# Performance work log

Measured on AMD Instinct MI355X. Metric: run time of the kernel, lower is better.

The kernel has to match this reference:

```python
import jax
import jax.numpy as jnp
import numpy as np

SIGMA = 0.5
COLLISION_WEIGHT = 100.0
CE_WEIGHTS = (1.0, 30.0, 30.0, 10.0)
B, V, F, P = 512, 778, 1538, 1024


def _cone_field(tri, pts):
    # Conical distance field of receiver triangle `tri` [B,P,3,3] evaluated at
    # intruder vertices `pts` [B,P,3,3] (Tzionas et al. penetration field,
    # penalize_outside=False, point2plane=False). Returns [B,P].
    c = tri.mean(axis=-2)                                   # triangle center [B,P,3]
    n = jnp.cross(tri[..., 1, :] - tri[..., 0, :], tri[..., 2, :] - tri[..., 0, :])
    n = n / (jnp.linalg.norm(n, axis=-1, keepdims=True) + 1e-9)
    d = pts - c[..., None, :]                               # [B,P,3,3]
    h = jnp.einsum('bpvc,bpc->bpv', d, n)                   # signed height along normal
    rho2 = jnp.maximum(jnp.sum(d * d, axis=-1) - h * h, 0.0)  # squared radial dist
    phi = jax.nn.relu(-h) * jnp.exp(-rho2 / (2.0 * SIGMA * SIGMA))
    return phi.sum(axis=-1)


def _pen_distance(triangles, collision_idxs):
    # triangles [B,2F,3,3]; collision_idxs [B,P,2] with -1 padding -> per-batch loss [B]
    bb = jnp.arange(triangles.shape[0])[:, None]
    valid = (collision_idxs[..., 0] >= 0) & (collision_idxs[..., 1] >= 0)
    idx = jnp.maximum(collision_idxs, 0)
    recv = triangles[bb, idx[..., 0]]                       # [B,P,3,3]
    intr = triangles[bb, idx[..., 1]]
    pair = _cone_field(recv, intr) + _cone_field(intr, recv)
    return jnp.sum(pair * valid, axis=1)


def _collision_loss(out_vertices, faces, collision_idxs):
    nv = out_vertices.shape[2]
    verts = jnp.concatenate([out_vertices[0], out_vertices[1]], axis=1)   # [B,2V,3]
    faces_comb = jnp.concatenate([faces[0], faces[1] + nv], axis=0)       # [2F,3]
    triangles = verts[:, faces_comb]                                      # [B,2F,3,3]
    loss_b = _pen_distance(triangles, collision_idxs)
    nz = (loss_b != 0).astype(loss_b.dtype)
    cnt = nz.sum()
    return jnp.where(cnt > 0, (loss_b * nz).sum() / jnp.maximum(cnt, 1.0) * COLLISION_WEIGHT, 0.0)


def _index_loss(elem, mask):
    # masked mean exactly as Loss.index_losss: sum(loss*mask)/ (mask.sum()*D), 0 if empty
    l = elem.reshape(elem.shape[0], -1)
    denom = mask.sum() * l.shape[1]
    return jnp.where(denom > 0, (l * mask[:, None]).sum() / jnp.maximum(denom, 1.0), 0.0)


def _mse(a, b):
    return (a - b) ** 2


def _l1(a, b):
    return jnp.abs(a - b)


def setup_inputs():
    key = jax.random.key(0)
    ks = jax.random.split(key, 20)
    f32 = jnp.float32
    out_vertices = jax.random.normal(ks[0], (2, B, V, 3), f32) * 0.05
    out_betas = jax.random.normal(ks[1], (2, B, 10), f32)
    out_transl = jax.random.normal(ks[2], (2, B, 3), f32) * 0.1
    out_j3d = jax.random.normal(ks[3], (2, B, 21, 3), f32) * 0.1
    out_go = jax.random.normal(ks[4], (2, B, 3), f32)
    out_pose = jax.random.normal(ks[5], (2, B, 45), f32)
    tgt_trans = jax.random.normal(ks[6], (2, B, 3), f32) * 0.1
    tgt_j3d = jax.random.normal(ks[7], (2, B, 21, 3), f32) * 0.1
    tgt_go = jax.random.normal(ks[8], (2, B, 3), f32)
    tgt_pose = jax.random.normal(ks[9], (2, B, 45), f32)
    tgt_shape = jax.random.normal(ks[10], (2, B, 10), f32)
    class_logits = jax.random.normal(ks[11], (B, 4), f32)
    faces = jax.random.randint(ks[12], (2, F, 3), 0, V, jnp.int32)
    ci = jax.random.randint(ks[13], (B, P, 2), 0, 2 * F, jnp.int32)
    keep = jax.random.uniform(ks[14], (B, P, 1)) < 0.7
    collision_idxs = jnp.where(keep, ci, -1)
    handedness = jax.random.randint(ks[15], (B, 2), 0, 2, jnp.int32)
    valid = jax.random.randint(ks[16], (2, B), 0, 2, jnp.int32)
    class_targets = jax.random.randint(ks[17], (B,), 0, 4, jnp.int32)
    return dict(out_vertices=out_vertices, out_betas=out_betas, out_transl=out_transl,
                out_j3d=out_j3d, out_go=out_go, out_pose=out_pose, tgt_trans=tgt_trans,
                tgt_j3d=tgt_j3d, tgt_go=tgt_go, tgt_pose=tgt_pose, tgt_shape=tgt_shape,
                class_logits=class_logits, faces=faces, collision_idxs=collision_idxs,
                handedness=handedness, valid=valid, class_targets=class_targets)


def reference(out_vertices, out_betas, out_transl, out_j3d, out_go, out_pose,
              tgt_trans, tgt_j3d, tgt_go, tgt_pose, tgt_shape, class_logits,
              faces, collision_idxs, handedness, valid, class_targets):
    f32 = out_vertices.dtype
    loss_interpen = _collision_loss(out_vertices, faces, collision_idxs)
    inter = (handedness.sum(axis=1) == 2).astype(f32)
    loss_inter_shape = _index_loss(_mse(out_betas[0], out_betas[1]), inter)
    loss_inter_transl = _index_loss(_mse(out_transl[0] - out_transl[1],
                                         tgt_trans[0] - tgt_trans[1]), inter) * 100.0
    loss_inter_j3d = _index_loss(_mse(out_j3d[0] - out_j3d[1],
                                      tgt_j3d[0] - tgt_j3d[1]), inter) * 100.0
    lgo = lhp = lrj = lj3 = lsh = ltr = reg = jnp.zeros((), f32)
    for h in range(2):  # left, right
        m = valid[h].astype(f32)
        lgo = lgo + _index_loss(_mse(out_go[h], tgt_go[h]), m) * 10.0
        lhp = lhp + _index_loss(_mse(out_pose[h], tgt_pose[h]), m) * 10.0
        lrj = lrj + _index_loss(_l1((out_j3d[h][:, 1:] - out_j3d[h][:, :1]) * 1000.0,
                                    (tgt_j3d[h][:, 1:] - tgt_j3d[h][:, :1]) * 1000.0), m) * 0.01
        lj3 = lj3 + _index_loss(_l1(out_j3d[h] * 1000.0, tgt_j3d[h] * 1000.0), m) * 0.01
        lsh = lsh + _index_loss(_mse(out_betas[h], tgt_shape[h]), m) * 10.0
        ltr = ltr + _index_loss(_l1(out_transl[h], tgt_trans[h]), m) * 10.0
        reg = reg + 0.1 * _index_loss(_mse(out_betas[h], out_betas[h]), m)
        reg = reg + _index_loss(_mse(out_pose[h], out_pose[h]), m)
    # weighted cross entropy with ignore_index=0 (torch semantics)
    logp = jax.nn.log_softmax(class_logits, axis=-1)
    nll = -jnp.take_along_axis(logp, class_targets[:, None], axis=1)[:, 0]
    w = jnp.asarray(CE_WEIGHTS, f32)[class_targets]
    vmask = (class_targets != 0).astype(f32)
    ce = jnp.sum(w * vmask * nll) / jnp.maximum(jnp.sum(w * vmask), 1e-9)
    return jnp.stack([loss_interpen, loss_inter_shape, loss_inter_transl, loss_inter_j3d,
                      lgo, lhp, lrj, lj3, lsh, ltr, reg, ce])
```

## Files before the change

### kernel.cpp

```cpp
#include <hip/hip_runtime.h>
#include <math.h>

#define BB 512
#define VV 778
#define FF 1538
#define PP 1024
#define NS 16
#define TPB 512

__device__ __forceinline__ float cone3(const float3 t[3], const float3 p[3]) {
    const float third = 1.0f / 3.0f;
    float cx = (t[0].x + t[1].x + t[2].x) * third;
    float cy = (t[0].y + t[1].y + t[2].y) * third;
    float cz = (t[0].z + t[1].z + t[2].z) * third;
    float e1x = t[1].x - t[0].x, e1y = t[1].y - t[0].y, e1z = t[1].z - t[0].z;
    float e2x = t[2].x - t[0].x, e2y = t[2].y - t[0].y, e2z = t[2].z - t[0].z;
    float nx = e1y * e2z - e1z * e2y;
    float ny = e1z * e2x - e1x * e2z;
    float nz = e1x * e2y - e1y * e2x;
    float inv = 1.0f / (sqrtf(nx * nx + ny * ny + nz * nz) + 1e-9f);
    nx *= inv; ny *= inv; nz *= inv;
    float s = 0.0f;
#pragma unroll
    for (int i = 0; i < 3; i++) {
        float dx = p[i].x - cx, dy = p[i].y - cy, dz = p[i].z - cz;
        float h = dx * nx + dy * ny + dz * nz;
        float r2 = fmaxf(dx * dx + dy * dy + dz * dz - h * h, 0.0f);
        float rl = fmaxf(-h, 0.0f);
        s += rl * expf(-2.0f * r2);
    }
    return s;
}

__global__ __launch_bounds__(TPB) void per_batch_kernel(
    const float* __restrict__ verts,
    const int*   __restrict__ faces,
    const int*   __restrict__ cidx,
    const float* __restrict__ betas,
    const float* __restrict__ transl,
    const float* __restrict__ j3d,
    const float* __restrict__ go,
    const float* __restrict__ pose,
    const float* __restrict__ tgt_trans,
    const float* __restrict__ tgt_j3d,
    const float* __restrict__ tgt_go,
    const float* __restrict__ tgt_pose,
    const float* __restrict__ tgt_shape,
    float* __restrict__ ws)
{
    __shared__ float4 sv4[2 * VV];
    __shared__ int    sfc[2 * FF * 3];
    __shared__ float  red[TPB / 64][NS];
    const int b = blockIdx.x, tid = threadIdx.x;

    const float* v0 = verts + (size_t)b * VV * 3;
    const float* v1 = verts + (size_t)(BB + b) * VV * 3;
    float* svf = (float*)sv4;
    for (int i = tid; i < VV * 3; i += TPB) {
        int v = i / 3, c = i - v * 3;
        svf[(v << 2) + c]          = v0[i];
        svf[((VV + v) << 2) + c]   = v1[i];
    }
    for (int i = tid; i < 2 * FF * 3; i += TPB) sfc[i] = faces[i];
    __syncthreads();

    float part[NS];
#pragma unroll
    for (int k = 0; k < NS; k++) part[k] = 0.0f;

    const int2* ci = (const int2*)cidx + (size_t)b * PP;
    for (int p = tid; p < PP; p += TPB) {
        int2 fp = ci[p];
        if (fp.x < 0 || fp.y < 0) continue;
        float3 r[3], q[3];
        {
            int off = (fp.x >= FF) ? VV : 0;
            const int* f = sfc + fp.x * 3;
#pragma unroll
            for (int k = 0; k < 3; k++) {
                float4 w = sv4[f[k] + off];
                r[k] = make_float3(w.x, w.y, w.z);
            }
        }
        {
            int off = (fp.y >= FF) ? VV : 0;
            const int* f = sfc + fp.y * 3;
#pragma unroll
            for (int k = 0; k < 3; k++) {
                float4 w = sv4[f[k] + off];
                q[k] = make_float3(w.x, w.y, w.z);
            }
        }
        part[0] += cone3(r, q) + cone3(q, r);
    }

    if (tid < 63) {
        const int t = tid;
        if (t < 10) { float d = betas[b * 10 + t] - betas[(BB + b) * 10 + t]; part[1] = d * d; }
        if (t < 3) {
            float d = (transl[b * 3 + t] - transl[(BB + b) * 3 + t]) -
                      (tgt_trans[b * 3 + t] - tgt_trans[(BB + b) * 3 + t]);
            part[2] = d * d;
        }
        {
            float d = (j3d[b * 63 + t] - j3d[(BB + b) * 63 + t]) -
                      (tgt_j3d[b * 63 + t] - tgt_j3d[(BB + b) * 63 + t]);
            part[3] = d * d;
        }
#pragma unroll
        for (int h = 0; h < 2; h++) {
            const int base = 4 + 6 * h;
            const size_t ob = (size_t)(h * BB + b);
            if (t < 3)  { float d = go[ob * 3 + t] - tgt_go[ob * 3 + t]; part[base + 0] = d * d; }
            if (t < 45) { float d = pose[ob * 45 + t] - tgt_pose[ob * 45 + t]; part[base + 1] = d * d; }
            if (t < 60) {
                int j = 1 + t / 3, c = t % 3;
                float a  = (j3d[ob * 63 + j * 3 + c]     - j3d[ob * 63 + c]) * 1000.0f;
                float b2 = (tgt_j3d[ob * 63 + j * 3 + c] - tgt_j3d[ob * 63 + c]) * 1000.0f;
                part[base + 2] = fabsf(a - b2);
            }
            {
                float a = j3d[ob * 63 + t] * 1000.0f, b2 = tgt_j3d[ob * 63 + t] * 1000.0f;
                part[base + 3] = fabsf(a - b2);
            }
            if (t < 10) { float d = betas[ob * 10 + t] - tgt_shape[ob * 10 + t]; part[base + 4] = d * d; }
            if (t < 3)  { float d = transl[ob * 3 + t] - tgt_trans[ob * 3 + t]; part[base + 5] = fabsf(d); }
        }
    }

#pragma unroll
    for (int off = 32; off >= 1; off >>= 1) {
#pragma unroll
        for (int k = 0; k < NS; k++) part[k] += __shfl_down(part[k], off);
    }
    const int wave = tid >> 6, lane = tid & 63;
    if (lane == 0) {
#pragma unroll
        for (int k = 0; k < NS; k++) red[wave][k] = part[k];
    }
    __syncthreads();
    if (tid < NS) {
        float s = 0.0f;
#pragma unroll
        for (int w = 0; w < TPB / 64; w++) s += red[w][tid];
        ws[b * NS + tid] = s;
    }
}

__global__ __launch_bounds__(256) void finalize_kernel(
    const float* __restrict__ ws,
    const int*   __restrict__ handed,
    const int*   __restrict__ validm,
    const float* __restrict__ logits,
    const int*   __restrict__ ctgt,
    float* __restrict__ out)
{
    const int tid = threadIdx.x;
    const int NA = 22;
    float acc[22];
#pragma unroll
    for (int k = 0; k < NA; k++) acc[k] = 0.0f;

    for (int b = tid; b < BB; b += 256) {
        const float* w = ws + b * NS;
        float lb = w[0];
        acc[0] += lb;
        acc[1] += (lb != 0.0f) ? 1.0f : 0.0f;
        float inter = ((handed[b * 2] + handed[b * 2 + 1]) == 2) ? 1.0f : 0.0f;
        acc[2] += inter * w[1];
        acc[3] += inter * w[2];
        acc[4] += inter * w[3];
        acc[5] += inter;
#pragma unroll
        for (int h = 0; h < 2; h++) {
            float vm = (float)validm[h * BB + b];
            const int ab = 6 + 7 * h;
#pragma unroll
            for (int k = 0; k < 6; k++) acc[ab + k] += vm * w[4 + 6 * h + k];
            acc[ab + 6] += vm;
        }
        float l0 = logits[b * 4 + 0], l1 = logits[b * 4 + 1];
        float l2 = logits[b * 4 + 2], l3 = logits[b * 4 + 3];
        float m = fmaxf(fmaxf(l0, l1), fmaxf(l2, l3));
        float lse = m + logf(expf(l0 - m) + expf(l1 - m) + expf(l2 - m) + expf(l3 - m));
        int t = ctgt[b];
        float lt = (t == 0) ? l0 : (t == 1) ? l1 : (t == 2) ? l2 : l3;
        float nll = lse - lt;
        float cw = (t == 0) ? 1.0f : (t == 3) ? 10.0f : 30.0f;
        float vm = (t != 0) ? 1.0f : 0.0f;
        acc[20] += cw * vm * nll;
        acc[21] += cw * vm;
    }

#pragma unroll
    for (int off = 32; off >= 1; off >>= 1) {
#pragma unroll
        for (int k = 0; k < NA; k++) acc[k] += __shfl_down(acc[k], off);
    }
    __shared__ float red[4][22];
    const int wave = tid >> 6, lane = tid & 63;
    if (lane == 0) {
#pragma unroll
        for (int k = 0; k < NA; k++) red[wave][k] = acc[k];
    }
    __syncthreads();

    if (tid == 0) {
        float s[22];
#pragma unroll
        for (int k = 0; k < NA; k++)
            s[k] = red[0][k] + red[1][k] + red[2][k] + red[3][k];

        auto idxloss = [](float num, float cnt, float K) -> float {
            float denom = cnt * K;
            return (denom > 0.0f) ? num / fmaxf(denom, 1.0f) : 0.0f;
        };

        out[0] = (s[1] > 0.0f) ? s[0] / fmaxf(s[1], 1.0f) * 100.0f : 0.0f;
        out[1] = idxloss(s[2], s[5], 10.0f);
        out[2] = idxloss(s[3], s[5], 3.0f) * 100.0f;
        out[3] = idxloss(s[4], s[5], 63.0f) * 100.0f;
        out[4] = (idxloss(s[6],  s[12], 3.0f)  + idxloss(s[13], s[19], 3.0f))  * 10.0f;
        out[5] = (idxloss(s[7],  s[12], 45.0f) + idxloss(s[14], s[19], 45.0f)) * 10.0f;
        out[6] = (idxloss(s[8],  s[12], 60.0f) + idxloss(s[15], s[19], 60.0f)) * 0.01f;
        out[7] = (idxloss(s[9],  s[12], 63.0f) + idxloss(s[16], s[19], 63.0f)) * 0.01f;
        out[8] = (idxloss(s[10], s[12], 10.0f) + idxloss(s[17], s[19], 10.0f)) * 10.0f;
        out[9] = (idxloss(s[11], s[12], 3.0f)  + idxloss(s[18], s[19], 3.0f))  * 10.0f;
        out[10] = 0.0f;
        out[11] = s[20] / fmaxf(s[21], 1e-9f);
    }
}

extern "C" void kernel_launch(void* const* d_in, const int* in_sizes, int n_in,
                              void* d_out, int out_size, void* d_ws, size_t ws_size,
                              hipStream_t stream) {
    const float* verts   = (const float*)d_in[0];
    const float* betas   = (const float*)d_in[1];
    const float* transl  = (const float*)d_in[2];
    const float* j3d     = (const float*)d_in[3];
    const float* go      = (const float*)d_in[4];
    const float* pose    = (const float*)d_in[5];
    const float* tt      = (const float*)d_in[6];
    const float* tj      = (const float*)d_in[7];
    const float* tg      = (const float*)d_in[8];
    const float* tp      = (const float*)d_in[9];
    const float* tsh     = (const float*)d_in[10];
    const float* logits  = (const float*)d_in[11];
    const int*   faces   = (const int*)d_in[12];
    const int*   cidx    = (const int*)d_in[13];
    const int*   handed  = (const int*)d_in[14];
    const int*   validm  = (const int*)d_in[15];
    const int*   ctgt    = (const int*)d_in[16];
    float*       ws      = (float*)d_ws;
    float*       out     = (float*)d_out;

    per_batch_kernel<<<BB, TPB, 0, stream>>>(verts, faces, cidx, betas, transl,
                                             j3d, go, pose, tt, tj, tg, tp, tsh, ws);
    finalize_kernel<<<1, 256, 0, stream>>>(ws, handed, validm, logits, ctgt, out);
}
```

Before: 106.9 us.

## Use 1024-thread blocks with one pair per thread and split reductions

The block size doubles to 1024 so each thread handles exactly one collision pair without a loop. The 16-way shuffle reduction across all waves is replaced by a single-value reduction for the collision term, plus a 15-value reduction done only in wave 0 for the small per-batch losses. This cuts register pressure and shuffle work in most waves. The trade-off is that the larger block may limit occupancy, since each block also holds about 61 KB of shared memory, and the shared-memory staging loops now have more threads.

```diff
diff --git a/kernel.cpp b/kernel.cpp
--- a/kernel.cpp
+++ b/kernel.cpp
@@ -6,7 +6,7 @@
 #define FF 1538
 #define PP 1024
 #define NS 16
-#define TPB 512
+#define TPB 1024
 
 __device__ __forceinline__ float cone3(const float3 t[3], const float3 p[3]) {
     const float third = 1.0f / 3.0f;
@@ -50,7 +50,7 @@
 {
     __shared__ float4 sv4[2 * VV];
     __shared__ int    sfc[2 * FF * 3];
-    __shared__ float  red[TPB / 64][NS];
+    __shared__ float  redc[TPB / 64];
     const int b = blockIdx.x, tid = threadIdx.x;
 
     const float* v0 = verts + (size_t)b * VV * 3;
@@ -58,92 +58,96 @@
     float* svf = (float*)sv4;
     for (int i = tid; i < VV * 3; i += TPB) {
         int v = i / 3, c = i - v * 3;
-        svf[(v << 2) + c]          = v0[i];
-        svf[((VV + v) << 2) + c]   = v1[i];
+        svf[(v << 2) + c]        = v0[i];
+        svf[((VV + v) << 2) + c] = v1[i];
     }
     for (int i = tid; i < 2 * FF * 3; i += TPB) sfc[i] = faces[i];
     __syncthreads();
 
-    float part[NS];
-#pragma unroll
-    for (int k = 0; k < NS; k++) part[k] = 0.0f;
-
-    const int2* ci = (const int2*)cidx + (size_t)b * PP;
-    for (int p = tid; p < PP; p += TPB) {
-        int2 fp = ci[p];
-        if (fp.x < 0 || fp.y < 0) continue;
-        float3 r[3], q[3];
-        {
-            int off = (fp.x >= FF) ? VV : 0;
-            const int* f = sfc + fp.x * 3;
-#pragma unroll
-            for (int k = 0; k < 3; k++) {
-                float4 w = sv4[f[k] + off];
-                r[k] = make_float3(w.x, w.y, w.z);
-            }
-        }
-        {
-            int off = (fp.y >= FF) ? VV : 0;
-            const int* f = sfc + fp.y * 3;
-#pragma unroll
-            for (int k = 0; k < 3; k++) {
-                float4 w = sv4[f[k] + off];
-                q[k] = make_float3(w.x, w.y, w.z);
-            }
-        }
-        part[0] += cone3(r, q) + cone3(q, r);
-    }
-
-    if (tid < 63) {
-        const int t = tid;
-        if (t < 10) { float d = betas[b * 10 + t] - betas[(BB + b) * 10 + t]; part[1] = d * d; }
-        if (t < 3) {
-            float d = (transl[b * 3 + t] - transl[(BB + b) * 3 + t]) -
-                      (tgt_trans[b * 3 + t] - tgt_trans[(BB + b) * 3 + t]);
-            part[2] = d * d;
-        }
-        {
-            float d = (j3d[b * 63 + t] - j3d[(BB + b) * 63 + t]) -
-                      (tgt_j3d[b * 63 + t] - tgt_j3d[(BB + b) * 63 + t]);
-            part[3] = d * d;
-        }
-#pragma unroll
-        for (int h = 0; h < 2; h++) {
-            const int base = 4 + 6 * h;
-            const size_t ob = (size_t)(h * BB + b);
-            if (t < 3)  { float d = go[ob * 3 + t] - tgt_go[ob * 3 + t]; part[base + 0] = d * d; }
-            if (t < 45) { float d = pose[ob * 45 + t] - tgt_pose[ob * 45 + t]; part[base + 1] = d * d; }
-            if (t < 60) {
-                int j = 1 + t / 3, c = t % 3;
-                float a  = (j3d[ob * 63 + j * 3 + c]     - j3d[ob * 63 + c]) * 1000.0f;
-                float b2 = (tgt_j3d[ob * 63 + j * 3 + c] - tgt_j3d[ob * 63 + c]) * 1000.0f;
-                part[base + 2] = fabsf(a - b2);
-            }
+    float col = 0.0f;
+    {
+        int2 fp = ((const int2*)cidx)[(size_t)b * PP + tid];
+        if (fp.x >= 0 && fp.y >= 0) {
+            float3 r[3], q[3];
             {
-                float a = j3d[ob * 63 + t] * 1000.0f, b2 = tgt_j3d[ob * 63 + t] * 1000.0f;
-                part[base + 3] = fabsf(a - b2);
-            }
-            if (t < 10) { float d = betas[ob * 10 + t] - tgt_shape[ob * 10 + t]; part[base + 4] = d * d; }
-            if (t < 3)  { float d = transl[ob * 3 + t] - tgt_trans[ob * 3 + t]; part[base + 5] = fabsf(d); }
-        }
-    }
-
-#pragma unroll
-    for (int off = 32; off >= 1; off >>= 1) {
-#pragma unroll
-        for (int k = 0; k < NS; k++) part[k] += __shfl_down(part[k], off);
-    }
+                int off = (fp.x >= FF) ? VV : 0;
+                const int* f = sfc + fp.x * 3;
+#pragma unroll
+                for (int k = 0; k < 3; k++) {
+                    float4 w = sv4[f[k] + off];
+                    r[k] = make_float3(w.x, w.y, w.z);
+                }
+            }
+            {
+                int off = (fp.y >= FF) ? VV : 0;
+                const int* f = sfc + fp.y * 3;
+#pragma unroll
+                for (int k = 0; k < 3; k++) {
+                    float4 w = sv4[f[k] + off];
+                    q[k] = make_float3(w.x, w.y, w.z);
+                }
+            }
+            col = cone3(r, q) + cone3(q, r);
+        }
+    }
+#pragma unroll
+    for (int off = 32; off >= 1; off >>= 1) col += __shfl_down(col, off);
     const int wave = tid >> 6, lane = tid & 63;
-    if (lane == 0) {
-#pragma unroll
-        for (int k = 0; k < NS; k++) red[wave][k] = part[k];
+    if (lane == 0) redc[wave] = col;
+
+    if (wave == 0) {
+        float sm[15];
+#pragma unroll
+        for (int k = 0; k < 15; k++) sm[k] = 0.0f;
+        if (lane < 63) {
+            const int t = lane;
+            if (t < 10) { float d = betas[b * 10 + t] - betas[(BB + b) * 10 + t]; sm[0] = d * d; }
+            if (t < 3) {
+                float d = (transl[b * 3 + t] - transl[(BB + b) * 3 + t]) -
+                          (tgt_trans[b * 3 + t] - tgt_trans[(BB + b) * 3 + t]);
+                sm[1] = d * d;
+            }
+            {
+                float d = (j3d[b * 63 + t] - j3d[(BB + b) * 63 + t]) -
+                          (tgt_j3d[b * 63 + t] - tgt_j3d[(BB + b) * 63 + t]);
+                sm[2] = d * d;
+            }
+#pragma unroll
+            for (int h = 0; h < 2; h++) {
+                const int base = 3 + 6 * h;
+                const size_t ob = (size_t)(h * BB + b);
+                if (t < 3)  { float d = go[ob * 3 + t] - tgt_go[ob * 3 + t]; sm[base + 0] = d * d; }
+                if (t < 45) { float d = pose[ob * 45 + t] - tgt_pose[ob * 45 + t]; sm[base + 1] = d * d; }
+                if (t < 60) {
+                    int j = 1 + t / 3, c = t % 3;
+                    float a  = (j3d[ob * 63 + j * 3 + c]     - j3d[ob * 63 + c]) * 1000.0f;
+                    float b2 = (tgt_j3d[ob * 63 + j * 3 + c] - tgt_j3d[ob * 63 + c]) * 1000.0f;
+                    sm[base + 2] = fabsf(a - b2);
+                }
+                {
+                    float a = j3d[ob * 63 + t] * 1000.0f, b2 = tgt_j3d[ob * 63 + t] * 1000.0f;
+                    sm[base + 3] = fabsf(a - b2);
+                }
+                if (t < 10) { float d = betas[ob * 10 + t] - tgt_shape[ob * 10 + t]; sm[base + 4] = d * d; }
+                if (t < 3)  { float d = transl[ob * 3 + t] - tgt_trans[ob * 3 + t]; sm[base + 5] = fabsf(d); }
+            }
+        }
+#pragma unroll
+        for (int off = 32; off >= 1; off >>= 1) {
+#pragma unroll
+            for (int k = 0; k < 15; k++) sm[k] += __shfl_down(sm[k], off);
+        }
+        if (lane == 0) {
+#pragma unroll
+            for (int k = 0; k < 15; k++) ws[b * NS + 1 + k] = sm[k];
+        }
     }
     __syncthreads();
-    if (tid < NS) {
+    if (tid == 0) {
         float s = 0.0f;
 #pragma unroll
-        for (int w = 0; w < TPB / 64; w++) s += red[w][tid];
-        ws[b * NS + tid] = s;
+        for (int w = 0; w < TPB / 64; w++) s += redc[w];
+        ws[b * NS] = s;
     }
 }
 
```

Result: no change. 105.8 us (-1.1%).
